# Optimization experiments

Measured on AMD Instinct MI355X. Metric: run time of the kernel, lower is better.

The kernel has to match this reference:

```python
import math
import jax, jax.numpy as jnp
import numpy as np

SIZE = 4096
ROWS = 16384


def fwht(x):
    """Fast Walsh-Hadamard transform along the last axis (Sylvester ordering).
    x: (..., n) with n a power of 2. Equivalent to x @ H_n (unnormalized)."""
    n = x.shape[-1]
    pre = x.shape[:-1]
    h = 2
    while h <= n:
        # group last axis into blocks of size h; butterfly across the two halves
        x = x.reshape(pre + (n // h, 2, h // 2))
        a = x[..., 0, :]
        b = x[..., 1, :]
        x = jnp.concatenate([a + b, a - b], axis=-1)  # (..., n//h, h)
        h *= 2
    return x.reshape(pre + (n,))


def setup_inputs() -> dict:
    key = jax.random.key(0)
    kx, ks = jax.random.split(key)
    x = jax.random.normal(kx, (ROWS, SIZE), dtype=jnp.float32)
    # original: Rademacher +-1 signs; sign pattern irrelevant for correctness math
    s = jnp.where(jax.random.uniform(ks, (SIZE,)) < 0.5, -1.0, 1.0).astype(jnp.float32)
    return {"x": x, "s": s}


def reference(x, s):
    # out = hadamard_transform(s * x) * scale, scale = 1/sqrt(2^ceil(log2(size)))
    scale = 1.0 / math.sqrt(2 ** math.ceil(math.log2(SIZE)))
    return fwht(s * x) * scale
```

## Files before the change

### kernel.cpp

```cpp
#include <hip/hip_runtime.h>

#define FWHT_SIZE 4096
#define TPB 256

__device__ __forceinline__ void fwht16(float a[16]) {
#pragma unroll
    for (int h = 1; h < 16; h <<= 1) {
#pragma unroll
        for (int i = 0; i < 16; i += 2 * h) {
#pragma unroll
            for (int j = i; j < i + h; ++j) {
                float u = a[j];
                float v = a[j + h];
                a[j]     = u + v;
                a[j + h] = u - v;
            }
        }
    }
}

#define LDS_WORDS 4368

__global__ __launch_bounds__(TPB, 8) void fwht_rows_kernel(
        const float* __restrict__ x,
        const float* __restrict__ s,
        float* __restrict__ out) {
    __shared__ float lds[LDS_WORDS];

    const int row = blockIdx.x;
    const int t   = threadIdx.x;
    const float* xr = x   + (size_t)row * FWHT_SIZE;
    float*       orw = out + (size_t)row * FWHT_SIZE;

    float a[16];

    {
        const float4* xv = (const float4*)(xr + 16 * t);
        const float4* sv = (const float4*)(s + 16 * t);
#pragma unroll
        for (int j = 0; j < 4; ++j) {
            float4 xx = xv[j];
            float4 ss = sv[j];
            a[4 * j + 0] = xx.x * ss.x;
            a[4 * j + 1] = xx.y * ss.y;
            a[4 * j + 2] = xx.z * ss.z;
            a[4 * j + 3] = xx.w * ss.w;
        }
    }
    fwht16(a);

    {
        const int base = 17 * t + (t >> 4);
#pragma unroll
        for (int j = 0; j < 16; ++j) lds[base + j] = a[j];
    }
    __syncthreads();

    const int hi = t >> 4;
    const int lo = t & 15;

    {
        const int base = 273 * hi + lo;
#pragma unroll
        for (int k = 0; k < 16; ++k) a[k] = lds[base + 17 * k];
    }
    fwht16(a);
    {
        const int base = 273 * hi + lo;
#pragma unroll
        for (int k = 0; k < 16; ++k) lds[base + 17 * k] = a[k];
    }
    __syncthreads();

    {
        const int base = 17 * hi + lo;
#pragma unroll
        for (int k = 0; k < 16; ++k) a[k] = lds[base + 273 * k];
    }
    fwht16(a);

    const float scale = 0.015625f;
#pragma unroll
    for (int k = 0; k < 16; ++k) {
        orw[256 * k + t] = a[k] * scale;
    }
}

extern "C" void kernel_launch(void* const* d_in, const int* in_sizes, int n_in,
                              void* d_out, int out_size, void* d_ws, size_t ws_size,
                              hipStream_t stream) {
    const float* x = (const float*)d_in[0];
    const float* s = (const float*)d_in[1];
    float* out = (float*)d_out;
    const int rows = in_sizes[0] / FWHT_SIZE;
    fwht_rows_kernel<<<rows, TPB, 0, stream>>>(x, s, out);
}
```

Measured before the change: 423.5 us.

## Restructure FWHT index decomposition with coalesced float4 loads and XOR-swizzled LDS

Changes how the 4096-point transform is split across the three radix-16 stages. Each thread now loads strided float4 chunks (4*t + 1024*k), so global reads are fully coalesced across the wavefront instead of each thread reading 64 contiguous bytes. The LDS padding is replaced by an XOR swizzle, which allows vectorized float4 LDS stores, shrinks LDS use, and is meant to avoid bank conflicts. The launch_bounds occupancy hint is also removed, which changes the register and occupancy constraints the compiler works under.

```diff
diff --git a/kernel.cpp b/kernel.cpp
--- a/kernel.cpp
+++ b/kernel.cpp
@@ -1,6 +1,6 @@
 #include <hip/hip_runtime.h>
 
-#define FWHT_SIZE 4096
+#define FWHT_N 4096
 #define TPB 256
 
 __device__ __forceinline__ void fwht16(float a[16]) {
@@ -19,9 +19,9 @@
     }
 }
 
-#define LDS_WORDS 4368
+#define LDS_WORDS 4096
 
-__global__ __launch_bounds__(TPB, 8) void fwht_rows_kernel(
+__global__ __launch_bounds__(TPB) void fwht_rows_kernel(
         const float* __restrict__ x,
         const float* __restrict__ s,
         float* __restrict__ out) {
@@ -29,60 +29,56 @@
 
     const int row = blockIdx.x;
     const int t   = threadIdx.x;
-    const float* xr = x   + (size_t)row * FWHT_SIZE;
-    float*       orw = out + (size_t)row * FWHT_SIZE;
+    const float* xr  = x   + (size_t)row * FWHT_N;
+    float*       orw = out + (size_t)row * FWHT_N;
 
     float a[16];
 
-    {
-        const float4* xv = (const float4*)(xr + 16 * t);
-        const float4* sv = (const float4*)(s + 16 * t);
 #pragma unroll
-        for (int j = 0; j < 4; ++j) {
-            float4 xx = xv[j];
-            float4 ss = sv[j];
-            a[4 * j + 0] = xx.x * ss.x;
-            a[4 * j + 1] = xx.y * ss.y;
-            a[4 * j + 2] = xx.z * ss.z;
-            a[4 * j + 3] = xx.w * ss.w;
-        }
+    for (int k = 0; k < 4; ++k) {
+        float4 xx = *(const float4*)(xr + 4 * t + 1024 * k);
+        float4 ss = *(const float4*)(s  + 4 * t + 1024 * k);
+        a[4 * k + 0] = xx.x * ss.x;
+        a[4 * k + 1] = xx.y * ss.y;
+        a[4 * k + 2] = xx.z * ss.z;
+        a[4 * k + 3] = xx.w * ss.w;
     }
     fwht16(a);
 
-    {
-        const int base = 17 * t + (t >> 4);
 #pragma unroll
-        for (int j = 0; j < 16; ++j) lds[base + j] = a[j];
-    }
-    __syncthreads();
-
-    const int hi = t >> 4;
-    const int lo = t & 15;
-
-    {
-        const int base = 273 * hi + lo;
-#pragma unroll
-        for (int k = 0; k < 16; ++k) a[k] = lds[base + 17 * k];
-    }
-    fwht16(a);
-    {
-        const int base = 273 * hi + lo;
-#pragma unroll
-        for (int k = 0; k < 16; ++k) lds[base + 17 * k] = a[k];
+    for (int k = 0; k < 4; ++k) {
+        int i    = 4 * t + 1024 * k;
+        int addr = i ^ (((i >> 6) & 15) << 2);
+        *(float4*)(lds + addr) =
+            make_float4(a[4 * k + 0], a[4 * k + 1], a[4 * k + 2], a[4 * k + 3]);
     }
     __syncthreads();
 
     {
-        const int base = 17 * hi + lo;
+        const int w    = t >> 2;
+        const int base = 64 * w + (t & 3);
+        const int swz  = w & 15;
 #pragma unroll
-        for (int k = 0; k < 16; ++k) a[k] = lds[base + 273 * k];
+        for (int m = 0; m < 16; ++m) a[m] = lds[base + 4 * (m ^ swz)];
+        fwht16(a);
+#pragma unroll
+        for (int m = 0; m < 16; ++m) lds[base + 4 * (m ^ swz)] = a[m];
+    }
+    __syncthreads();
+
+    {
+        const int hi = 1024 * (t >> 6);
+        const int lo = t & 63;
+#pragma unroll
+        for (int m = 0; m < 16; ++m) a[m] = lds[hi + 64 * m + (lo ^ (m << 2))];
     }
     fwht16(a);
 
     const float scale = 0.015625f;
+    const int baseO = (t & 63) + 1024 * (t >> 6);
 #pragma unroll
-    for (int k = 0; k < 16; ++k) {
-        orw[256 * k + t] = a[k] * scale;
+    for (int m = 0; m < 16; ++m) {
+        orw[baseO + 64 * m] = a[m] * scale;
     }
 }
 
@@ -92,6 +88,6 @@
     const float* x = (const float*)d_in[0];
     const float* s = (const float*)d_in[1];
     float* out = (float*)d_out;
-    const int rows = in_sizes[0] / FWHT_SIZE;
+    const int rows = in_sizes[0] / FWHT_N;
     fwht_rows_kernel<<<rows, TPB, 0, stream>>>(x, s, out);
 }
```

Result: no change. 422.0 us (-0.3%).
